# Kernel optimization log

Measured on AMD Instinct MI355X. Metric: run time of the kernel, lower is better.

The kernel has to match this reference:

```python
import jax, jax.numpy as jnp
import numpy as np

B, T, D_IN, NB = 8, 4096, 128, 32  # batch, frames, in_dim, n_basis
STRIDE = 2


def setup_inputs() -> dict:
    key = jax.random.key(0)
    kx, ke, kf = jax.random.split(key, 3)
    std = np.sqrt(2.0 / (D_IN + NB)).astype(np.float32)
    return {
        "X": jax.random.normal(kx, (B, T, D_IN), dtype=jnp.float32),
        "E": jax.random.normal(ke, (D_IN, NB), dtype=jnp.float32) * std,
        "F": jax.random.normal(kf, (D_IN, NB), dtype=jnp.float32) * std,
        "G": jnp.ones((1,), dtype=jnp.float32),
        "bx": jnp.zeros((NB,), dtype=jnp.float32),
        "by": jnp.zeros((NB,), dtype=jnp.float32),
    }


def reference(X, E, F, G, bx, by):
    # z1, z2: [B, T, NB]
    z1 = jnp.einsum("btd,dn->btn", X, E) + bx
    z2 = jnp.einsum("btd,dn->btn", X, F) + by
    # per-frame outer product -> [B, T, NB*NB], scaled by G
    z = G[0] * (z1[..., :, None] * z2[..., None, :]).reshape(B, T, NB * NB)
    # AveragePooling1D(pool_size=stride, strides=stride, padding='same');
    # T divisible by STRIDE so 'same' adds no padding.
    out_pool = z.reshape(B, T // STRIDE, STRIDE, NB * NB).mean(axis=2)
    return out_pool
```

## Files before the change

### kernel.cpp

```cpp
#include <hip/hip_runtime.h>


#define DIN 128
#define NB_ 32

constexpr int FR   = 64;
constexpr int SXS  = 132;
constexpr int SWS  = 68;
constexpr int SZS  = 68;
constexpr int NBLK = (8 * 4096) / FR;

__global__ __launch_bounds__(128) void trp_fused(
    const float* __restrict__ X, const float* __restrict__ E,
    const float* __restrict__ F, const float* __restrict__ G,
    const float* __restrict__ bx, const float* __restrict__ by,
    float* __restrict__ out)
{
    __shared__ __align__(16) float sw[DIN * SWS];
    __shared__ __align__(16) float sxz[FR * SXS];

    const int tid = threadIdx.x;
    const int blk = blockIdx.x;

    #pragma unroll
    for (int it = 0; it < 16; ++it) {
        int v = tid + 128 * it;
        int d = v >> 4, c = v & 15;
        const float* src = (c < 8) ? (E + d * NB_ + c * 4)
                                   : (F + d * NB_ + (c - 8) * 4);
        *(float4*)&sw[d * SWS + c * 4] = *(const float4*)src;
    }
    const float* xb = X + (size_t)blk * FR * DIN;
    #pragma unroll
    for (int it = 0; it < 16; ++it) {
        int v = tid + 128 * it;
        int f = v >> 5, dc = v & 31;
        *(float4*)&sxz[f * SXS + dc * 4] = *(const float4*)(xb + f * DIN + dc * 4);
    }
    __syncthreads();

    const int wave = tid >> 6;
    const int n0   = (tid & 15) * 4;
    const int fg   = (tid >> 4) & 3;
    const int fA   = wave * 16 + fg * 4;

    float acc[2][4][4];
    #pragma unroll
    for (int cl = 0; cl < 2; ++cl)
        #pragma unroll
        for (int q = 0; q < 4; ++q)
            #pragma unroll
            for (int c = 0; c < 4; ++c) acc[cl][q][c] = 0.f;

    #pragma unroll 2
    for (int dc = 0; dc < DIN / 4; ++dc) {
        const int d4 = dc * 4;
        float w[4][4];
        #pragma unroll
        for (int r = 0; r < 4; ++r)
            *(float4*)&w[r][0] = *(const float4*)&sw[(d4 + r) * SWS + n0];
        #pragma unroll
        for (int cl = 0; cl < 2; ++cl) {
            #pragma unroll
            for (int q = 0; q < 4; ++q) {
                float x[4];
                *(float4*)&x[0] = *(const float4*)&sxz[(fA + cl * 32 + q) * SXS + d4];
                #pragma unroll
                for (int r = 0; r < 4; ++r)
                    #pragma unroll
                    for (int c = 0; c < 4; ++c)
                        acc[cl][q][c] = fmaf(x[r], w[r][c], acc[cl][q][c]);
            }
        }
    }

    float bias[4], scale;
    if (n0 < NB_) { *(float4*)bias = *(const float4*)(bx + n0);       scale = 0.5f * G[0]; }
    else          { *(float4*)bias = *(const float4*)(by + n0 - NB_); scale = 1.0f; }

    #pragma unroll
    for (int cl = 0; cl < 2; ++cl) {
        const int zb = (cl * 32 + wave * 16) * SXS;
        #pragma unroll
        for (int q = 0; q < 4; ++q) {
            float4 z;
            z.x = (acc[cl][q][0] + bias[0]) * scale;
            z.y = (acc[cl][q][1] + bias[1]) * scale;
            z.z = (acc[cl][q][2] + bias[2]) * scale;
            z.w = (acc[cl][q][3] + bias[3]) * scale;
            *(float4*)&sxz[zb + (fg * 4 + q) * SZS + n0] = z;
        }
    }
    __syncthreads();

    const int lane = tid & 63;
    const int j4 = lane & 7;
    const int i0 = lane >> 3;
    float4* out4 = (float4*)out;
    const int pooledBase = blk * 32;

    #pragma unroll
    for (int cl = 0; cl < 2; ++cl) {
        const int zb = (cl * 32 + wave * 16) * SXS;
        const int pfBase = pooledBase + cl * 16 + wave * 8;
        #pragma unroll 2
        for (int pp = 0; pp < 8; ++pp) {
            const float* zr0 = &sxz[zb + (2 * pp) * SZS];
            const float* zr1 = zr0 + SZS;
            float4 v0 = *(const float4*)&zr0[NB_ + 4 * j4];
            float4 v1 = *(const float4*)&zr1[NB_ + 4 * j4];
            float4* ob = out4 + (size_t)(pfBase + pp) * 256 + lane;
            #pragma unroll
            for (int t = 0; t < 4; ++t) {
                const int i = i0 + 8 * t;
                float a0 = zr0[i];
                float a1 = zr1[i];
                float4 r;
                r.x = fmaf(a0, v0.x, a1 * v1.x);
                r.y = fmaf(a0, v0.y, a1 * v1.y);
                r.z = fmaf(a0, v0.z, a1 * v1.z);
                r.w = fmaf(a0, v0.w, a1 * v1.w);
                ob[64 * t] = r;
            }
        }
    }
}

extern "C" void kernel_launch(void* const* d_in, const int* in_sizes, int n_in,
                              void* d_out, int out_size, void* d_ws, size_t ws_size,
                              hipStream_t stream) {
    const float* X  = (const float*)d_in[0];
    const float* E  = (const float*)d_in[1];
    const float* F  = (const float*)d_in[2];
    const float* G  = (const float*)d_in[3];
    const float* bx = (const float*)d_in[4];
    const float* by = (const float*)d_in[5];
    float* outp = (float*)d_out;
    trp_fused<<<dim3(NBLK), dim3(128), 0, stream>>>(X, E, F, G, bx, by, outp);
}
```

Before: 112.4 us.

## Double threads per block, halve per-thread frames, drop second barrier

Result: faster. 109.8 us (-2.3%).

```diff
diff --git a/kernel.cpp b/kernel.cpp
--- a/kernel.cpp
+++ b/kernel.cpp
@@ -6,51 +6,52 @@
 
 constexpr int FR   = 64;
 constexpr int SXS  = 132;
-constexpr int SWS  = 68;
-constexpr int SZS  = 68;
 constexpr int NBLK = (8 * 4096) / FR;
 
-__global__ __launch_bounds__(128) void trp_fused(
+__global__ __launch_bounds__(256) void trp_fused(
     const float* __restrict__ X, const float* __restrict__ E,
     const float* __restrict__ F, const float* __restrict__ G,
     const float* __restrict__ bx, const float* __restrict__ by,
     float* __restrict__ out)
 {
-    __shared__ __align__(16) float sw[DIN * SWS];
+    __shared__ __align__(16) float sw[DIN * 64];
     __shared__ __align__(16) float sxz[FR * SXS];
 
     const int tid = threadIdx.x;
     const int blk = blockIdx.x;
 
+    const int n0 = (tid & 15) * 4;
+    float bias[4], scale;
+    if (n0 < NB_) { *(float4*)bias = *(const float4*)(bx + n0);       scale = 0.5f * G[0]; }
+    else          { *(float4*)bias = *(const float4*)(by + n0 - NB_); scale = 1.0f; }
+    float bs[4];
     #pragma unroll
-    for (int it = 0; it < 16; ++it) {
-        int v = tid + 128 * it;
+    for (int c = 0; c < 4; ++c) bs[c] = bias[c] * scale;
+
+    #pragma unroll
+    for (int it = 0; it < 8; ++it) {
+        int v = tid + 256 * it;
         int d = v >> 4, c = v & 15;
         const float* src = (c < 8) ? (E + d * NB_ + c * 4)
                                    : (F + d * NB_ + (c - 8) * 4);
-        *(float4*)&sw[d * SWS + c * 4] = *(const float4*)src;
+        *(float4*)&sw[d * 64 + c * 4] = *(const float4*)src;
     }
     const float* xb = X + (size_t)blk * FR * DIN;
     #pragma unroll
-    for (int it = 0; it < 16; ++it) {
-        int v = tid + 128 * it;
+    for (int it = 0; it < 8; ++it) {
+        int v = tid + 256 * it;
         int f = v >> 5, dc = v & 31;
         *(float4*)&sxz[f * SXS + dc * 4] = *(const float4*)(xb + f * DIN + dc * 4);
     }
     __syncthreads();
 
-    const int wave = tid >> 6;
-    const int n0   = (tid & 15) * 4;
-    const int fg   = (tid >> 4) & 3;
-    const int fA   = wave * 16 + fg * 4;
+    const int f0 = (tid >> 4) * 4;
 
-    float acc[2][4][4];
+    float acc[4][4];
     #pragma unroll
-    for (int cl = 0; cl < 2; ++cl)
+    for (int q = 0; q < 4; ++q)
         #pragma unroll
-        for (int q = 0; q < 4; ++q)
-            #pragma unroll
-            for (int c = 0; c < 4; ++c) acc[cl][q][c] = 0.f;
+        for (int c = 0; c < 4; ++c) acc[q][c] = 0.f;
 
     #pragma unroll 2
     for (int dc = 0; dc < DIN / 4; ++dc) {
@@ -58,70 +59,54 @@
         float w[4][4];
         #pragma unroll
         for (int r = 0; r < 4; ++r)
-            *(float4*)&w[r][0] = *(const float4*)&sw[(d4 + r) * SWS + n0];
+            *(float4*)&w[r][0] = *(const float4*)&sw[(d4 + r) * 64 + n0];
         #pragma unroll
-        for (int cl = 0; cl < 2; ++cl) {
+        for (int q = 0; q < 4; ++q) {
+            float x[4];
+            *(float4*)&x[0] = *(const float4*)&sxz[(f0 + q) * SXS + d4];
             #pragma unroll
-            for (int q = 0; q < 4; ++q) {
-                float x[4];
-                *(float4*)&x[0] = *(const float4*)&sxz[(fA + cl * 32 + q) * SXS + d4];
+            for (int r = 0; r < 4; ++r)
                 #pragma unroll
-                for (int r = 0; r < 4; ++r)
-                    #pragma unroll
-                    for (int c = 0; c < 4; ++c)
-                        acc[cl][q][c] = fmaf(x[r], w[r][c], acc[cl][q][c]);
-            }
+                for (int c = 0; c < 4; ++c)
+                    acc[q][c] = fmaf(x[r], w[r][c], acc[q][c]);
         }
     }
 
-    float bias[4], scale;
-    if (n0 < NB_) { *(float4*)bias = *(const float4*)(bx + n0);       scale = 0.5f * G[0]; }
-    else          { *(float4*)bias = *(const float4*)(by + n0 - NB_); scale = 1.0f; }
+    #pragma unroll
+    for (int q = 0; q < 4; ++q) {
+        float4 z;
+        z.x = fmaf(acc[q][0], scale, bs[0]);
+        z.y = fmaf(acc[q][1], scale, bs[1]);
+        z.z = fmaf(acc[q][2], scale, bs[2]);
+        z.w = fmaf(acc[q][3], scale, bs[3]);
+        *(float4*)&sxz[(f0 + q) * SXS + n0] = z;
+    }
 
-    #pragma unroll
-    for (int cl = 0; cl < 2; ++cl) {
-        const int zb = (cl * 32 + wave * 16) * SXS;
-        #pragma unroll
-        for (int q = 0; q < 4; ++q) {
-            float4 z;
-            z.x = (acc[cl][q][0] + bias[0]) * scale;
-            z.y = (acc[cl][q][1] + bias[1]) * scale;
-            z.z = (acc[cl][q][2] + bias[2]) * scale;
-            z.w = (acc[cl][q][3] + bias[3]) * scale;
-            *(float4*)&sxz[zb + (fg * 4 + q) * SZS + n0] = z;
-        }
-    }
-    __syncthreads();
-
+    const int wave = tid >> 6;
     const int lane = tid & 63;
     const int j4 = lane & 7;
     const int i0 = lane >> 3;
     float4* out4 = (float4*)out;
-    const int pooledBase = blk * 32;
+    const int pfBase = blk * 32 + wave * 8;
 
-    #pragma unroll
-    for (int cl = 0; cl < 2; ++cl) {
-        const int zb = (cl * 32 + wave * 16) * SXS;
-        const int pfBase = pooledBase + cl * 16 + wave * 8;
-        #pragma unroll 2
-        for (int pp = 0; pp < 8; ++pp) {
-            const float* zr0 = &sxz[zb + (2 * pp) * SZS];
-            const float* zr1 = zr0 + SZS;
-            float4 v0 = *(const float4*)&zr0[NB_ + 4 * j4];
-            float4 v1 = *(const float4*)&zr1[NB_ + 4 * j4];
-            float4* ob = out4 + (size_t)(pfBase + pp) * 256 + lane;
-            #pragma unroll
-            for (int t = 0; t < 4; ++t) {
-                const int i = i0 + 8 * t;
-                float a0 = zr0[i];
-                float a1 = zr1[i];
-                float4 r;
-                r.x = fmaf(a0, v0.x, a1 * v1.x);
-                r.y = fmaf(a0, v0.y, a1 * v1.y);
-                r.z = fmaf(a0, v0.z, a1 * v1.z);
-                r.w = fmaf(a0, v0.w, a1 * v1.w);
-                ob[64 * t] = r;
-            }
+    #pragma unroll 2
+    for (int pp = 0; pp < 8; ++pp) {
+        const float* zr0 = &sxz[(wave * 16 + 2 * pp) * SXS];
+        const float* zr1 = zr0 + SXS;
+        float4 v0 = *(const float4*)&zr0[NB_ + 4 * j4];
+        float4 v1 = *(const float4*)&zr1[NB_ + 4 * j4];
+        float4* ob = out4 + (size_t)(pfBase + pp) * 256 + lane;
+        #pragma unroll
+        for (int t = 0; t < 4; ++t) {
+            const int i = i0 + 8 * t;
+            float a0 = zr0[i];
+            float a1 = zr1[i];
+            float4 r;
+            r.x = fmaf(a0, v0.x, a1 * v1.x);
+            r.y = fmaf(a0, v0.y, a1 * v1.y);
+            r.z = fmaf(a0, v0.z, a1 * v1.z);
+            r.w = fmaf(a0, v0.w, a1 * v1.w);
+            ob[64 * t] = r;
         }
     }
 }
@@ -136,5 +121,5 @@
     const float* bx = (const float*)d_in[4];
     const float* by = (const float*)d_in[5];
     float* outp = (float*)d_out;
-    trp_fused<<<dim3(NBLK), dim3(128), 0, stream>>>(X, E, F, G, bx, by, outp);
+    trp_fused<<<dim3(NBLK), dim3(256), 0, stream>>>(X, E, F, G, bx, by, outp);
 }
```
